# Optimization experiments

Measured on AMD Instinct MI355X. Metric: run time of the kernel, lower is better.

## Reference

```python
import jax, jax.numpy as jnp
import numpy as np

B, L, D, H = 4, 2048, 1024, 16
HD = D // H
EPS_LN = 1e-12
EPS_Z = 1e-6


def _rope_tables(seq_len, d_model, base=10000.0):
    k_max = d_model // 2
    theta = 1.0 / (base ** (np.arange(k_max, dtype=np.float32) / k_max))
    ang = np.arange(seq_len, dtype=np.float32)[:, None] * theta[None, :]  # [L, D/2]
    return jnp.asarray(np.cos(ang)), jnp.asarray(np.sin(ang))


def _apply_rope(x, cos, sin):
    # x: [B, L, D]; complex rotation on (even, odd) pairs of last dim
    xr, xi = x[..., 0::2], x[..., 1::2]          # [B, L, D/2]
    or_ = xr * cos - xi * sin
    oi = xr * sin + xi * cos
    return jnp.stack([or_, oi], axis=-1).reshape(x.shape)


def _layernorm(x, g, b):
    mu = jnp.mean(x, axis=-1, keepdims=True)
    var = jnp.mean(jnp.square(x - mu), axis=-1, keepdims=True)
    return (x - mu) * jax.lax.rsqrt(var + EPS_LN) * g + b


def _heads(t):
    # [B, L, D] -> [B, H, L, HD]
    return t.reshape(B, L, H, HD).transpose(0, 2, 1, 3)


def _attn(x, W_qk, b_qk, conv_w, conv_b, cos, sin):
    # x: [B, L, D] (output of in_proj)
    qk = x @ W_qk + b_qk                                  # [B, L, 2D]
    q = jax.nn.elu(qk[..., :D]) + 1.0
    k = jax.nn.elu(qk[..., D:]) + 1.0
    v = x
    q_rope = _heads(_apply_rope(q, cos, sin))             # [B, H, L, HD]
    k_rope = _heads(_apply_rope(k, cos, sin))
    qh, kh, vh = _heads(q), _heads(k), _heads(v)
    # normalizer: 1 / (q . mean_L(k))
    k_mean = jnp.mean(kh, axis=2)                          # [B, H, HD]
    z = 1.0 / (jnp.einsum('bhld,bhd->bhl', qh, k_mean) + EPS_Z)  # [B, H, L]
    # kv accumulation (global, scaled by 1/L via two L^-0.5 factors)
    kv = jnp.einsum('bhld,bhle->bhde', k_rope, vh) / L     # [B, H, HD, HD]
    out = jnp.einsum('bhld,bhde->bhle', q_rope, kv) * z[..., None]  # [B,H,L,HD]
    out = out.transpose(0, 2, 1, 3).reshape(B, L, D)
    # depthwise causal conv + SiLU on v (left pad k-1=3, keep length L)
    v_t = v.transpose(0, 2, 1)                             # [B, D, L]
    conv = jax.lax.conv_general_dilated(
        v_t, conv_w, window_strides=(1,), padding=[(3, 0)],
        dimension_numbers=('NCH', 'OIH', 'NCH'), feature_group_count=D)
    conv = jax.nn.silu(conv + conv_b[:, None])             # [B, D, L]
    return out + conv.transpose(0, 2, 1)


def setup_inputs() -> dict:
    key = jax.random.key(0)
    ks = jax.random.split(key, 12)
    s = 0.02
    return {
        'x': jax.random.normal(ks[0], (B, L, D), jnp.float32),
        'ln1_g': jnp.ones((D,), jnp.float32), 'ln1_b': jnp.zeros((D,), jnp.float32),
        'ln2_g': jnp.ones((D,), jnp.float32), 'ln2_b': jnp.zeros((D,), jnp.float32),
        'W_act': jax.random.normal(ks[1], (D, D), jnp.float32) * s,
        'b_act': jnp.zeros((D,), jnp.float32),
        'W_in': jax.random.normal(ks[2], (D, D), jnp.float32) * s,
        'b_in': jnp.zeros((D,), jnp.float32),
        'W_qk': jax.random.normal(ks[3], (D, 2 * D), jnp.float32) * s,
        'b_qk': jnp.zeros((2 * D,), jnp.float32),
        'conv_w': jax.random.normal(ks[4], (D, 1, 4), jnp.float32) * 0.25,
        'conv_b': jnp.zeros((D,), jnp.float32),
        'W_out': jax.random.normal(ks[5], (D, D), jnp.float32) * s,
        'b_out': jnp.zeros((D,), jnp.float32),
        'W1': jax.random.normal(ks[6], (D, 4 * D), jnp.float32) * s,
        'b1': jnp.zeros((4 * D,), jnp.float32),
        'W2': jax.random.normal(ks[7], (4 * D, D), jnp.float32) * s,
        'b2': jnp.zeros((D,), jnp.float32),
    }


def reference(x, ln1_g, ln1_b, ln2_g, ln2_b, W_act, b_act, W_in, b_in,
              W_qk, b_qk, conv_w, conv_b, W_out, b_out, W1, b1, W2, b2):
    cos, sin = _rope_tables(L, D)
    shortcut = x
    h = _layernorm(x, ln1_g, ln1_b)
    act_res = jax.nn.silu(h @ W_act + b_act)
    h = h @ W_in + b_in
    h = _attn(h, W_qk, b_qk, conv_w, conv_b, cos, sin)
    h = (h * act_res) @ W_out + b_out
    x = shortcut + h
    m = _layernorm(x, ln2_g, ln2_b)
    m = jax.nn.gelu(m @ W1 + b1, approximate=False) @ W2 + b2
    return x + m
```

## Files before the change

### kernel.cpp

```cpp
#include <hip/hip_runtime.h>
#include <math.h>

typedef unsigned short ushort_t;
typedef __attribute__((ext_vector_type(4))) float f32x4;
typedef __attribute__((ext_vector_type(8))) __bf16 bf16x8;
typedef __attribute__((ext_vector_type(8))) unsigned short u16x8;
typedef __attribute__((ext_vector_type(4))) unsigned short u16x4;

#define DEV __device__ __forceinline__

#define CB 4
#define CL 2048
#define CD 1024
#define CH 16
#define CHD 64
#define CM 8192

DEV float bf2f(ushort_t u) {
  unsigned int x = ((unsigned int)u) << 16;
  return __builtin_bit_cast(float, x);
}
DEV ushort_t f2bf(float f) {
  unsigned int u = __builtin_bit_cast(unsigned int, f);
  u += 0x7FFFu + ((u >> 16) & 1u);
  return (ushort_t)(u >> 16);
}
DEV void gload16(const void* g, void* l) {
  __builtin_amdgcn_global_load_lds((const __attribute__((address_space(1))) void*)g,
                                   (__attribute__((address_space(3))) void*)l, 16, 0, 0);
}
DEV bf16x8 frag64(const ushort_t* s, int row, int slog) {
  int sl = slog ^ (row & 7);
  return __builtin_bit_cast(bf16x8, *reinterpret_cast<const u16x8*>(s + row * 64 + sl * 8));
}

__global__ void k_rope_tables(ushort_t* __restrict__ cosT, ushort_t* __restrict__ sinT) {
  int idx = blockIdx.x * 256 + threadIdx.x;
  int l = idx >> 9, j = idx & 511;
  float theta = powf(10000.0f, -(float)j * (1.0f / 512.0f));
  float ang = (float)l * theta;
  float s, c;
  sincosf(ang, &s, &c);
  cosT[idx] = f2bf(c);
  sinT[idx] = f2bf(s);
}

__global__ void k_transpose_bf16(const float* __restrict__ src, ushort_t* __restrict__ dst,
                                 int R, int C) {
  __shared__ float tile[32][33];
  int c0 = blockIdx.x * 32, r0 = blockIdx.y * 32;
  int tx = threadIdx.x & 31, ty = threadIdx.x >> 5;
#pragma unroll
  for (int i = 0; i < 32; i += 8) tile[ty + i][tx] = src[(size_t)(r0 + ty + i) * C + c0 + tx];
  __syncthreads();
#pragma unroll
  for (int i = 0; i < 32; i += 8) dst[(size_t)(c0 + ty + i) * R + r0 + tx] = f2bf(tile[tx][ty + i]);
}

__global__ __launch_bounds__(256) void k_layernorm(const float* __restrict__ x,
                                                   const float* __restrict__ g,
                                                   const float* __restrict__ b,
                                                   ushort_t* __restrict__ out) {
  int row = blockIdx.x, t = threadIdx.x;
  const float* xr = x + (size_t)row * CD;
  f32x4 v = ((const f32x4*)xr)[t];
  float s = v.x + v.y + v.z + v.w;
  float s2 = v.x * v.x + v.y * v.y + v.z * v.z + v.w * v.w;
#pragma unroll
  for (int off = 32; off >= 1; off >>= 1) {
    s += __shfl_xor(s, off);
    s2 += __shfl_xor(s2, off);
  }
  __shared__ float red[8];
  int lane = t & 63, w = t >> 6;
  if (lane == 0) { red[w] = s; red[w + 4] = s2; }
  __syncthreads();
  s = red[0] + red[1] + red[2] + red[3];
  s2 = red[4] + red[5] + red[6] + red[7];
  float mu = s * (1.0f / CD);
  float var = s2 * (1.0f / CD) - mu * mu;
  float rs = rsqrtf(var + 1e-12f);
  f32x4 gg = ((const f32x4*)g)[t];
  f32x4 bb = ((const f32x4*)b)[t];
  u16x4 o;
  o.x = f2bf((v.x - mu) * rs * gg.x + bb.x);
  o.y = f2bf((v.y - mu) * rs * gg.y + bb.y);
  o.z = f2bf((v.z - mu) * rs * gg.z + bb.z);
  o.w = f2bf((v.w - mu) * rs * gg.w + bb.w);
  ((u16x4*)(out + (size_t)row * CD))[t] = o;
}

enum { EP_PLAIN = 0, EP_SILU = 1, EP_ELU1 = 2, EP_GELU = 3, EP_ADDX = 4 };

template <int EP>
__global__ __launch_bounds__(256, 2) void k_gemm(const ushort_t* __restrict__ A,
                                                 const ushort_t* __restrict__ Bt, int N, int K,
                                                 const float* __restrict__ bias,
                                                 const float* __restrict__ addf,
                                                 float* __restrict__ outf,
                                                 ushort_t* __restrict__ outb) {
  __shared__ __align__(16) ushort_t sA[128 * 64];
  __shared__ __align__(16) ushort_t sB[128 * 64];
  const int t = threadIdx.x;
  const int lane = t & 63;
  const int w = t >> 6;
  const int wr = w >> 1, wc = w & 1;
  const int m0 = blockIdx.y * 128, n0 = blockIdx.x * 128;

  f32x4 acc[4][4];
#pragma unroll
  for (int i = 0; i < 4; ++i)
#pragma unroll
    for (int j = 0; j < 4; ++j) acc[i][j] = f32x4{0.f, 0.f, 0.f, 0.f};

  for (int kt = 0; kt < K; kt += 64) {
#pragma unroll
    for (int i = 0; i < 4; ++i) {
      int c = t + i * 256;
      int row = c >> 3;
      int sl = (c & 7) ^ (row & 7);
      int ldsoff = (w * 64 + i * 256) * 8;
      gload16(A + (size_t)(m0 + row) * K + kt + sl * 8, sA + ldsoff);
      gload16(Bt + (size_t)(n0 + row) * K + kt + sl * 8, sB + ldsoff);
    }
    __syncthreads();
#pragma unroll
    for (int kk = 0; kk < 2; ++kk) {
      int slog = kk * 4 + (lane >> 4);
      bf16x8 af[4], bfr[4];
#pragma unroll
      for (int mi = 0; mi < 4; ++mi) af[mi] = frag64(sA, wr * 64 + mi * 16 + (lane & 15), slog);
#pragma unroll
      for (int ni = 0; ni < 4; ++ni) bfr[ni] = frag64(sB, wc * 64 + ni * 16 + (lane & 15), slog);
#pragma unroll
      for (int mi = 0; mi < 4; ++mi)
#pragma unroll
        for (int ni = 0; ni < 4; ++ni)
          acc[mi][ni] =
              __builtin_amdgcn_mfma_f32_16x16x32_bf16(af[mi], bfr[ni], acc[mi][ni], 0, 0, 0);
    }
    __syncthreads();
  }

#pragma unroll
  for (int mi = 0; mi < 4; ++mi) {
#pragma unroll
    for (int ni = 0; ni < 4; ++ni) {
      int col = n0 + wc * 64 + ni * 16 + (lane & 15);
      float bc = bias[col];
#pragma unroll
      for (int r = 0; r < 4; ++r) {
        int row = m0 + wr * 64 + mi * 16 + (lane >> 4) * 4 + r;
        size_t idx = (size_t)row * N + col;
        float vv = acc[mi][ni][r] + bc;
        if constexpr (EP == EP_PLAIN) {
          outb[idx] = f2bf(vv);
        } else if constexpr (EP == EP_SILU) {
          outb[idx] = f2bf(vv / (1.f + expf(-vv)));
        } else if constexpr (EP == EP_ELU1) {
          outb[idx] = f2bf(vv > 0.f ? vv + 1.f : expf(vv));
        } else if constexpr (EP == EP_GELU) {
          outb[idx] = f2bf(0.5f * vv * (1.f + erff(vv * 0.70710678118654752f)));
        } else {
          outf[idx] = addf[idx] + vv;
        }
      }
    }
  }
}

__global__ __launch_bounds__(256) void k_attn_reduce(const ushort_t* __restrict__ qk,
                                                     const ushort_t* __restrict__ vbf,
                                                     const ushort_t* __restrict__ cosT,
                                                     const ushort_t* __restrict__ sinT,
                                                     float* __restrict__ kvpart,
                                                     float* __restrict__ kmpart) {
  int bh = blockIdx.x >> 2, ls = blockIdx.x & 3;
  int b = bh >> 4, h = bh & 15;
  int t = threadIdx.x, lane = t & 63, w = t >> 6;

  __shared__ float kst[64][68];
  __shared__ __align__(16) ushort_t krT[64 * 64];
  __shared__ __align__(16) ushort_t vT[64 * 64];
  __shared__ float cst[64][32];
  __shared__ float snt[64][32];
  __shared__ float kmp[4][64];

  float kmacc = 0.f;
  f32x4 acc[4];
#pragma unroll
  for (int i = 0; i < 4; ++i) acc[i] = f32x4{0.f, 0.f, 0.f, 0.f};

  for (int c = ls * 8; c < ls * 8 + 8; ++c) {
    int l0 = c * 64;
    for (int idx = t; idx < 4096; idx += 256) {
      int l = idx >> 6, d = idx & 63;
      size_t grow = (size_t)(b * CL + l0 + l);
      float kvv = bf2f(qk[grow * 2048 + 1024 + h * 64 + d]);
      kst[l][d] = kvv;
      kmacc += kvv;
      ushort_t vv = vbf[grow * CD + h * 64 + d];
      int sl = (l >> 3) ^ (d & 7);
      vT[d * 64 + sl * 8 + (l & 7)] = vv;
    }
    for (int idx = t; idx < 2048; idx += 256) {
      int l = idx >> 5, j = idx & 31;
      size_t p = (size_t)(l0 + l) * 512 + h * 32 + j;
      cst[l][j] = bf2f(cosT[p]);
      snt[l][j] = bf2f(sinT[p]);
    }
    __syncthreads();
    for (int idx = t; idx < 4096; idx += 256) {
      int l = idx >> 6, d = idx & 63, j = d >> 1;
      float cc = cst[l][j], sn = snt[l][j];
      float kr = (d & 1) ? (kst[l][d - 1] * sn + kst[l][d] * cc)
                         : (kst[l][d] * cc - kst[l][d + 1] * sn);
      int sl = (l >> 3) ^ (d & 7);
      krT[d * 64 + sl * 8 + (l & 7)] = f2bf(kr);
    }
    __syncthreads();
#pragma unroll
    for (int kk = 0; kk < 2; ++kk) {
      int slog = kk * 4 + (lane >> 4);
      bf16x8 a = frag64(vT, w * 16 + (lane & 15), slog);
#pragma unroll
      for (int ni = 0; ni < 4; ++ni) {
        bf16x8 bb = frag64(krT, ni * 16 + (lane & 15), slog);
        acc[ni] = __builtin_amdgcn_mfma_f32_16x16x32_bf16(a, bb, acc[ni], 0, 0, 0);
      }
    }
    __syncthreads();
  }
  float* kp = kvpart + ((size_t)(bh * 4 + ls)) * 4096;
#pragma unroll
  for (int ni = 0; ni < 4; ++ni) {
    int d = ni * 16 + (lane & 15);
#pragma unroll
    for (int r = 0; r < 4; ++r) {
      int e = w * 16 + (lane >> 4) * 4 + r;
      kp[e * 64 + d] = acc[ni][r];
    }
  }
  kmp[t >> 6][t & 63] = kmacc;
  __syncthreads();
  if (t < 64) kmpart[(bh * 4 + ls) * 64 + t] = kmp[0][t] + kmp[1][t] + kmp[2][t] + kmp[3][t];
}

__global__ void k_kv_reduce(const float* __restrict__ kvpart, const float* __restrict__ kmpart,
                            ushort_t* __restrict__ kvT, float* __restrict__ kmean) {
  int gid = blockIdx.x * 256 + threadIdx.x;
  int bh = gid >> 12, r = gid & 4095;
  float s = 0.f;
#pragma unroll
  for (int ls = 0; ls < 4; ++ls) s += kvpart[((size_t)(bh * 4 + ls)) * 4096 + r];
  kvT[gid] = f2bf(s);
  if (gid < 64 * 64) {
    int bh2 = gid >> 6, d = gid & 63;
    float m = 0.f;
#pragma unroll
    for (int ls = 0; ls < 4; ++ls) m += kmpart[(bh2 * 4 + ls) * 64 + d];
    kmean[gid] = m;
  }
}

__global__ __launch_bounds__(256) void k_attn_out(const ushort_t* __restrict__ qk,
                                                  const ushort_t* __restrict__ kvT,
                                                  const float* __restrict__ kmean,
                                                  const ushort_t* __restrict__ cosT,
                                                  const ushort_t* __restrict__ sinT,
                                                  float* __restrict__ outlin) {
  int bid = blockIdx.x;
  int bh = bid >> 5, lt = bid & 31;
  int b = bh >> 4, h = bh & 15;
  int l0 = lt * 64;
  int t = threadIdx.x, lane = t & 63, w = t >> 6;

  __shared__ float qst[64][68];
  __shared__ __align__(16) ushort_t qrT[64 * 64];
  __shared__ __align__(16) ushort_t kvs[64 * 64];
  __shared__ float cst[64][32];
  __shared__ float snt[64][32];
  __shared__ float kms[64];
  __shared__ float zrow[64];

  if (t < 64) kms[t] = kmean[bh * 64 + t];
  for (int idx = t; idx < 4096; idx += 256) {
    int l = idx >> 6, d = idx & 63;
    qst[l][d] = bf2f(qk[(size_t)(b * CL + l0 + l) * 2048 + h * 64 + d]);
    ushort_t kvv = kvT[(size_t)bh * 4096 + idx];
    int e = idx >> 6, dd = idx & 63;
    int sl = (dd >> 3) ^ (e & 7);
    kvs[e * 64 + sl * 8 + (dd & 7)] = kvv;
  }
  for (int idx = t; idx < 2048; idx += 256) {
    int l = idx >> 5, j = idx & 31;
    size_t p = (size_t)(l0 + l) * 512 + h * 32 + j;
    cst[l][j] = bf2f(cosT[p]);
    snt[l][j] = bf2f(sinT[p]);
  }
  __syncthreads();
  for (int idx = t; idx < 4096; idx += 256) {
    int l = idx >> 6, d = idx & 63, j = d >> 1;
    float cc = cst[l][j], sn = snt[l][j];
    float qr = (d & 1) ? (qst[l][d - 1] * sn + qst[l][d] * cc)
                       : (qst[l][d] * cc - qst[l][d + 1] * sn);
    int sl = (d >> 3) ^ (l & 7);
    qrT[l * 64 + sl * 8 + (d & 7)] = f2bf(qr);
  }
  if (t < 64) {
    float dot = 0.f;
#pragma unroll
    for (int d = 0; d < 64; ++d) dot += qst[t][d] * kms[d];
    zrow[t] = 1.0f / (dot * (1.0f / (float)CL) + 1e-6f);
  }
  __syncthreads();
  f32x4 acc[4];
#pragma unroll
  for (int i = 0; i < 4; ++i) acc[i] = f32x4{0.f, 0.f, 0.f, 0.f};
#pragma unroll
  for (int kk = 0; kk < 2; ++kk) {
    int slog = kk * 4 + (lane >> 4);
    bf16x8 a = frag64(qrT, w * 16 + (lane & 15), slog);
#pragma unroll
    for (int ni = 0; ni < 4; ++ni) {
      bf16x8 bb = frag64(kvs, ni * 16 + (lane & 15), slog);
      acc[ni] = __builtin_amdgcn_mfma_f32_16x16x32_bf16(a, bb, acc[ni], 0, 0, 0);
    }
  }
#pragma unroll
  for (int ni = 0; ni < 4; ++ni) {
    int e = ni * 16 + (lane & 15);
#pragma unroll
    for (int r = 0; r < 4; ++r) {
      int l = w * 16 + (lane >> 4) * 4 + r;
      float val = acc[ni][r] * zrow[l] * (1.0f / (float)CL);
      outlin[(size_t)(b * CL + l0 + l) * CD + h * 64 + e] = val;
    }
  }
}

__global__ void k_conv_mul(const float* __restrict__ outlin, const ushort_t* __restrict__ vbf,
                           const ushort_t* __restrict__ act, const float* __restrict__ convw,
                           const float* __restrict__ convb, ushort_t* __restrict__ A4) {
  int idx = blockIdx.x * 256 + threadIdx.x;
  int d = idx & 1023;
  int bl = idx >> 10;
  int l = bl & 2047;
  float accv = 0.f;
#pragma unroll
  for (int tt = 0; tt < 4; ++tt) {
    int ll = l - 3 + tt;
    if (ll >= 0) accv += bf2f(vbf[(size_t)(bl - 3 + tt) * CD + d]) * convw[d * 4 + tt];
  }
  accv += convb[d];
  accv = accv / (1.f + expf(-accv));
  float a4 = (outlin[idx] + accv) * bf2f(act[idx]);
  A4[idx] = f2bf(a4);
}

extern "C" void kernel_launch(void* const* d_in, const int* in_sizes, int n_in, void* d_out,
                              int out_size, void* d_ws, size_t ws_size, hipStream_t stream) {
  const float* x = (const float*)d_in[0];
  const float* ln1_g = (const float*)d_in[1];
  const float* ln1_b = (const float*)d_in[2];
  const float* ln2_g = (const float*)d_in[3];
  const float* ln2_b = (const float*)d_in[4];
  const float* W_act = (const float*)d_in[5];
  const float* b_act = (const float*)d_in[6];
  const float* W_in = (const float*)d_in[7];
  const float* b_in = (const float*)d_in[8];
  const float* W_qk = (const float*)d_in[9];
  const float* b_qk = (const float*)d_in[10];
  const float* conv_w = (const float*)d_in[11];
  const float* conv_b = (const float*)d_in[12];
  const float* W_out = (const float*)d_in[13];
  const float* b_out = (const float*)d_in[14];
  const float* W1 = (const float*)d_in[15];
  const float* b1 = (const float*)d_in[16];
  const float* W2 = (const float*)d_in[17];
  const float* b2 = (const float*)d_in[18];
  float* out = (float*)d_out;

  char* w = (char*)d_ws;
  size_t off = 0;
  auto alloc = [&](size_t bytes) {
    void* p = (void*)(w + off);
    off += (bytes + 255) & ~(size_t)255;
    return p;
  };
  const size_t MB = 1024 * 1024;
  ushort_t* cosT = (ushort_t*)alloc((size_t)CL * 512 * 2);
  ushort_t* sinT = (ushort_t*)alloc((size_t)CL * 512 * 2);
  ushort_t* WactT = (ushort_t*)alloc((size_t)1024 * 1024 * 2);
  ushort_t* WinT = (ushort_t*)alloc((size_t)1024 * 1024 * 2);
  ushort_t* WqkT = (ushort_t*)alloc((size_t)2048 * 1024 * 2);
  ushort_t* WoutT = (ushort_t*)alloc((size_t)1024 * 1024 * 2);
  ushort_t* W1T = (ushort_t*)alloc((size_t)4096 * 1024 * 2);
  ushort_t* W2T = (ushort_t*)alloc((size_t)1024 * 4096 * 2);
  ushort_t* kvTb = (ushort_t*)alloc((size_t)64 * 4096 * 2);
  float* kmean = (float*)alloc((size_t)64 * 64 * 4);
  float* kvpart = (float*)alloc((size_t)256 * 4096 * 4);
  float* kmpart = (float*)alloc((size_t)256 * 64 * 4);
  float* x2 = (float*)alloc((size_t)CM * CD * 4);
  char* R1 = (char*)alloc(64 * MB);
  ushort_t* hln = (ushort_t*)R1;
  ushort_t* qkb = (ushort_t*)(R1 + 16 * MB);
  ushort_t* actb = (ushort_t*)(R1 + 48 * MB);
  ushort_t* Gb = (ushort_t*)R1;
  ushort_t* vb = (ushort_t*)alloc(16 * MB);
  char* R2 = (char*)alloc(48 * MB);
  float* outlin = (float*)R2;
  ushort_t* A4 = (ushort_t*)(R2 + 32 * MB);
  ushort_t* mln = (ushort_t*)R2;

  (void)in_sizes; (void)n_in; (void)out_size; (void)ws_size;

  k_rope_tables<<<4096, 256, 0, stream>>>(cosT, sinT);
  k_transpose_bf16<<<dim3(32, 32), 256, 0, stream>>>(W_act, WactT, 1024, 1024);
  k_transpose_bf16<<<dim3(32, 32), 256, 0, stream>>>(W_in, WinT, 1024, 1024);
  k_transpose_bf16<<<dim3(64, 32), 256, 0, stream>>>(W_qk, WqkT, 1024, 2048);
  k_transpose_bf16<<<dim3(32, 32), 256, 0, stream>>>(W_out, WoutT, 1024, 1024);
  k_transpose_bf16<<<dim3(128, 32), 256, 0, stream>>>(W1, W1T, 1024, 4096);
  k_transpose_bf16<<<dim3(32, 128), 256, 0, stream>>>(W2, W2T, 4096, 1024);

  k_layernorm<<<CM, 256, 0, stream>>>(x, ln1_g, ln1_b, hln);

  k_gemm<EP_SILU><<<dim3(8, 64), 256, 0, stream>>>(hln, WactT, 1024, 1024, b_act, nullptr, nullptr, actb);
  k_gemm<EP_PLAIN><<<dim3(8, 64), 256, 0, stream>>>(hln, WinT, 1024, 1024, b_in, nullptr, nullptr, vb);
  k_gemm<EP_ELU1><<<dim3(16, 64), 256, 0, stream>>>(vb, WqkT, 2048, 1024, b_qk, nullptr, nullptr, qkb);

  k_attn_reduce<<<256, 256, 0, stream>>>(qkb, vb, cosT, sinT, kvpart, kmpart);
  k_kv_reduce<<<1024, 256, 0, stream>>>(kvpart, kmpart, kvTb, kmean);
  k_attn_out<<<2048, 256, 0, stream>>>(qkb, kvTb, kmean, cosT, sinT, outlin);
  k_conv_mul<<<32768, 256, 0, stream>>>(outlin, vb, actb, conv_w, conv_b, A4);

  k_gemm<EP_ADDX><<<dim3(8, 64), 256, 0, stream>>>(A4, WoutT, 1024, 1024, b_out, x, x2, nullptr);
  k_layernorm<<<CM, 256, 0, stream>>>(x2, ln2_g, ln2_b, mln);
  k_gemm<EP_GELU><<<dim3(32, 64), 256, 0, stream>>>(mln, W1T, 4096, 1024, b1, nullptr, nullptr, Gb);
  k_gemm<EP_ADDX><<<dim3(8, 64), 256, 0, stream>>>(Gb, W2T, 1024, 4096, b2, x2, out, nullptr);
}
```

Before: 493.4 us.

## Fuse act/in/qk GEMMs via precomposed weights and pipeline GEMM loads

Precomposes W_in·W_qk into a single weight and bias so the act, in and qk projections run as one N=4096 GEMM from the layernorm output, with a three-region epilogue (SiLU, plain, ELU+1). This removes the dependent qk GEMM that previously had to wait for the in_proj result. It also replaces the GEMM with a 512-thread 256x128 tile kernel that triple-buffers global-to-LDS loads using vmcnt waits, remaps block IDs into groups of eight, and raises wave priority during MFMA. The cost is an extra weight-composition GEMM in setup, and qk is now computed from a bf16 product of bf16 weights, which changes rounding relative to the two-step path.

Result: slower. 635.4 us (+28.8%).

```diff
diff --git a/kernel.cpp b/kernel.cpp
--- a/kernel.cpp
+++ b/kernel.cpp
@@ -12,8 +12,6 @@
 #define CB 4
 #define CL 2048
 #define CD 1024
-#define CH 16
-#define CHD 64
 #define CM 8192
 
 DEV float bf2f(ushort_t u) {
@@ -37,7 +35,7 @@
 __global__ void k_rope_tables(ushort_t* __restrict__ cosT, ushort_t* __restrict__ sinT) {
   int idx = blockIdx.x * 256 + threadIdx.x;
   int l = idx >> 9, j = idx & 511;
-  float theta = powf(10000.0f, -(float)j * (1.0f / 512.0f));
+  float theta = exp2f(-(float)j * (13.2877123795494f / 512.0f));
   float ang = (float)l * theta;
   float s, c;
   sincosf(ang, &s, &c);
@@ -55,6 +53,35 @@
   __syncthreads();
 #pragma unroll
   for (int i = 0; i < 32; i += 8) dst[(size_t)(c0 + ty + i) * R + r0 + tx] = f2bf(tile[tx][ty + i]);
+}
+
+__global__ void k_cast_bf16(const float* __restrict__ src, ushort_t* __restrict__ dst) {
+  int i = blockIdx.x * 256 + threadIdx.x;
+  f32x4 v = ((const f32x4*)src)[i];
+  u16x4 o;
+  o.x = f2bf(v.x); o.y = f2bf(v.y); o.z = f2bf(v.z); o.w = f2bf(v.w);
+  ((u16x4*)dst)[i] = o;
+}
+
+__global__ void k_prep_bias(const float* __restrict__ b_act, const float* __restrict__ b_in,
+                            const float* __restrict__ b_qk, const ushort_t* __restrict__ WqkT,
+                            float* __restrict__ bf) {
+  int n = blockIdx.x * 256 + threadIdx.x;
+  if (n < 1024) {
+    bf[n] = b_act[n];
+  } else if (n < 2048) {
+    bf[n] = b_in[n - 1024];
+  } else {
+    int np = n - 2048;
+    float s = b_qk[np];
+    const ushort_t* wr = WqkT + (size_t)np * 1024;
+    for (int j = 0; j < 1024; j += 8) {
+      u16x8 wv = *reinterpret_cast<const u16x8*>(wr + j);
+#pragma unroll
+      for (int k2 = 0; k2 < 8; ++k2) s += bf2f(wv[k2]) * b_in[j + k2];
+    }
+    bf[n] = s;
+  }
 }
 
 __global__ __launch_bounds__(256) void k_layernorm(const float* __restrict__ x,
@@ -90,22 +117,51 @@
   ((u16x4*)(out + (size_t)row * CD))[t] = o;
 }
 
-enum { EP_PLAIN = 0, EP_SILU = 1, EP_ELU1 = 2, EP_GELU = 3, EP_ADDX = 4 };
+enum { EP_PLAIN = 0, EP_GELU = 3, EP_ADDX = 4, EP_FUSED1 = 5 };
+
+#define STAGE6(kt_, b_)                                        \
+  {                                                            \
+    const int kt__ = (kt_);                                    \
+    const int bo__ = (b_) * 24576;                             \
+    _Pragma("unroll") for (int i_ = 0; i_ < 4; ++i_)           \
+        gload16(aSrc[i_] + kt__, aDst[i_] + bo__);             \
+    _Pragma("unroll") for (int i_ = 0; i_ < 2; ++i_)           \
+        gload16(bSrc[i_] + kt__, bDst[i_] + bo__);             \
+  }
 
 template <int EP>
-__global__ __launch_bounds__(256, 2) void k_gemm(const ushort_t* __restrict__ A,
-                                                 const ushort_t* __restrict__ Bt, int N, int K,
-                                                 const float* __restrict__ bias,
-                                                 const float* __restrict__ addf,
-                                                 float* __restrict__ outf,
-                                                 ushort_t* __restrict__ outb) {
-  __shared__ __align__(16) ushort_t sA[128 * 64];
-  __shared__ __align__(16) ushort_t sB[128 * 64];
+__global__ __launch_bounds__(512, 2) void k_gemm2(
+    const ushort_t* __restrict__ A, const ushort_t* __restrict__ Bt, int N, int K, int nbx,
+    const float* __restrict__ bias, const float* __restrict__ addf, float* __restrict__ outf,
+    ushort_t* __restrict__ outb, ushort_t* __restrict__ out2, ushort_t* __restrict__ out3) {
+  __shared__ __align__(16) ushort_t smem[3 * 24576];
   const int t = threadIdx.x;
-  const int lane = t & 63;
-  const int w = t >> 6;
+  const int lane = t & 63, w = t >> 6;
   const int wr = w >> 1, wc = w & 1;
-  const int m0 = blockIdx.y * 128, n0 = blockIdx.x * 128;
+  const int lr = lane & 15, lq = lane >> 4;
+
+  int bid = blockIdx.x;
+  int qq = gridDim.x >> 3;
+  int wg = (bid & 7) * qq + (bid >> 3);
+  int by = wg / nbx, bx = wg - by * nbx;
+  const int m0 = by << 8, n0 = bx << 7;
+
+  const ushort_t* aSrc[4];
+  ushort_t* aDst[4];
+#pragma unroll
+  for (int i = 0; i < 4; ++i) {
+    int c = t + i * 512, row = c >> 3, sl = (c & 7) ^ (row & 7);
+    aSrc[i] = A + (size_t)(m0 + row) * K + sl * 8;
+    aDst[i] = smem + (size_t)(w * 64 + i * 512) * 8;
+  }
+  const ushort_t* bSrc[2];
+  ushort_t* bDst[2];
+#pragma unroll
+  for (int i = 0; i < 2; ++i) {
+    int c = t + i * 512, row = c >> 3, sl = (c & 7) ^ (row & 7);
+    bSrc[i] = Bt + (size_t)(n0 + row) * K + sl * 8;
+    bDst[i] = smem + 16384 + (size_t)(w * 64 + i * 512) * 8;
+  }
 
   f32x4 acc[4][4];
 #pragma unroll
@@ -113,25 +169,31 @@
 #pragma unroll
     for (int j = 0; j < 4; ++j) acc[i][j] = f32x4{0.f, 0.f, 0.f, 0.f};
 
-  for (int kt = 0; kt < K; kt += 64) {
-#pragma unroll
-    for (int i = 0; i < 4; ++i) {
-      int c = t + i * 256;
-      int row = c >> 3;
-      int sl = (c & 7) ^ (row & 7);
-      int ldsoff = (w * 64 + i * 256) * 8;
-      gload16(A + (size_t)(m0 + row) * K + kt + sl * 8, sA + ldsoff);
-      gload16(Bt + (size_t)(n0 + row) * K + kt + sl * 8, sB + ldsoff);
-    }
-    __syncthreads();
+  const int NT = K >> 6;
+  STAGE6(0, 0);
+  STAGE6(64, 1);
+  for (int tt = 0; tt < NT; ++tt) {
+    if (tt + 2 < NT) {
+      STAGE6((tt + 2) << 6, (tt + 2) % 3);
+      asm volatile("s_waitcnt vmcnt(12)" ::: "memory");
+    } else if (tt + 1 < NT) {
+      asm volatile("s_waitcnt vmcnt(6)" ::: "memory");
+    } else {
+      asm volatile("s_waitcnt vmcnt(0)" ::: "memory");
+    }
+    __builtin_amdgcn_s_barrier();
+    __builtin_amdgcn_sched_barrier(0);
+    const ushort_t* sA = smem + (tt % 3) * 24576;
+    const ushort_t* sB = sA + 16384;
+    __builtin_amdgcn_s_setprio(1);
 #pragma unroll
     for (int kk = 0; kk < 2; ++kk) {
-      int slog = kk * 4 + (lane >> 4);
+      int slog = kk * 4 + lq;
       bf16x8 af[4], bfr[4];
 #pragma unroll
-      for (int mi = 0; mi < 4; ++mi) af[mi] = frag64(sA, wr * 64 + mi * 16 + (lane & 15), slog);
-#pragma unroll
-      for (int ni = 0; ni < 4; ++ni) bfr[ni] = frag64(sB, wc * 64 + ni * 16 + (lane & 15), slog);
+      for (int mi = 0; mi < 4; ++mi) af[mi] = frag64(sA, wr * 64 + mi * 16 + lr, slog);
+#pragma unroll
+      for (int ni = 0; ni < 4; ++ni) bfr[ni] = frag64(sB, wc * 64 + ni * 16 + lr, slog);
 #pragma unroll
       for (int mi = 0; mi < 4; ++mi)
 #pragma unroll
@@ -139,30 +201,37 @@
           acc[mi][ni] =
               __builtin_amdgcn_mfma_f32_16x16x32_bf16(af[mi], bfr[ni], acc[mi][ni], 0, 0, 0);
     }
-    __syncthreads();
-  }
-
+    __builtin_amdgcn_s_setprio(0);
+    __builtin_amdgcn_sched_barrier(0);
+    __builtin_amdgcn_s_barrier();
+  }
+
+  const int region = n0 >> 10;
 #pragma unroll
   for (int mi = 0; mi < 4; ++mi) {
 #pragma unroll
     for (int ni = 0; ni < 4; ++ni) {
-      int col = n0 + wc * 64 + ni * 16 + (lane & 15);
-      float bc = bias[col];
+      int col = n0 + wc * 64 + ni * 16 + lr;
+      float bc = bias ? bias[col] : 0.0f;
 #pragma unroll
       for (int r = 0; r < 4; ++r) {
-        int row = m0 + wr * 64 + mi * 16 + (lane >> 4) * 4 + r;
-        size_t idx = (size_t)row * N + col;
+        int row = m0 + wr * 64 + mi * 16 + lq * 4 + r;
         float vv = acc[mi][ni][r] + bc;
-        if constexpr (EP == EP_PLAIN) {
-          outb[idx] = f2bf(vv);
-        } else if constexpr (EP == EP_SILU) {
-          outb[idx] = f2bf(vv / (1.f + expf(-vv)));
-        } else if constexpr (EP == EP_ELU1) {
-          outb[idx] = f2bf(vv > 0.f ? vv + 1.f : expf(vv));
+        if constexpr (EP == EP_FUSED1) {
+          if (region == 0) {
+            outb[(size_t)row * 1024 + col] = f2bf(vv / (1.f + expf(-vv)));
+          } else if (region == 1) {
+            out2[(size_t)row * 1024 + (col - 1024)] = f2bf(vv);
+          } else {
+            out3[(size_t)row * 2048 + (col - 2048)] =
+                f2bf(vv > 0.f ? vv + 1.f : expf(vv));
+          }
+        } else if constexpr (EP == EP_PLAIN) {
+          outb[(size_t)row * N + col] = f2bf(vv);
         } else if constexpr (EP == EP_GELU) {
-          outb[idx] = f2bf(0.5f * vv * (1.f + erff(vv * 0.70710678118654752f)));
+          outb[(size_t)row * N + col] = f2bf(0.5f * vv * (1.f + erff(vv * 0.70710678118654752f)));
         } else {
-          outf[idx] = addf[idx] + vv;
+          outf[(size_t)row * N + col] = addf[(size_t)row * N + col] + vv;
         }
       }
     }
@@ -249,7 +318,8 @@
 __global__ void k_kv_reduce(const float* __restrict__ kvpart, const float* __restrict__ kmpart,
                             ushort_t* __restrict__ kvT, float* __restrict__ kmean) {
   int gid = blockIdx.x * 256 + threadIdx.x;
-  int bh = gid >> 12, r = gid & 4095;
+  int bh = gid >> 12;
+  int r = gid & 4095;
   float s = 0.f;
 #pragma unroll
   for (int ls = 0; ls < 4; ++ls) s += kvpart[((size_t)(bh * 4 + ls)) * 4096 + r];
@@ -391,9 +461,10 @@
   const size_t MB = 1024 * 1024;
   ushort_t* cosT = (ushort_t*)alloc((size_t)CL * 512 * 2);
   ushort_t* sinT = (ushort_t*)alloc((size_t)CL * 512 * 2);
-  ushort_t* WactT = (ushort_t*)alloc((size_t)1024 * 1024 * 2);
-  ushort_t* WinT = (ushort_t*)alloc((size_t)1024 * 1024 * 2);
+  ushort_t* WfT = (ushort_t*)alloc((size_t)4096 * 1024 * 2);
   ushort_t* WqkT = (ushort_t*)alloc((size_t)2048 * 1024 * 2);
+  ushort_t* WinB = (ushort_t*)alloc((size_t)1024 * 1024 * 2);
+  float* bfused = (float*)alloc((size_t)4096 * 4);
   ushort_t* WoutT = (ushort_t*)alloc((size_t)1024 * 1024 * 2);
   ushort_t* W1T = (ushort_t*)alloc((size_t)4096 * 1024 * 2);
   ushort_t* W2T = (ushort_t*)alloc((size_t)1024 * 4096 * 2);
@@ -416,26 +487,33 @@
   (void)in_sizes; (void)n_in; (void)out_size; (void)ws_size;
 
   k_rope_tables<<<4096, 256, 0, stream>>>(cosT, sinT);
-  k_transpose_bf16<<<dim3(32, 32), 256, 0, stream>>>(W_act, WactT, 1024, 1024);
-  k_transpose_bf16<<<dim3(32, 32), 256, 0, stream>>>(W_in, WinT, 1024, 1024);
   k_transpose_bf16<<<dim3(64, 32), 256, 0, stream>>>(W_qk, WqkT, 1024, 2048);
+  k_cast_bf16<<<1024, 256, 0, stream>>>(W_in, WinB);
+  k_transpose_bf16<<<dim3(32, 32), 256, 0, stream>>>(W_act, WfT, 1024, 1024);
+  k_transpose_bf16<<<dim3(32, 32), 256, 0, stream>>>(W_in, WfT + (size_t)1024 * 1024, 1024, 1024);
+  k_gemm2<EP_PLAIN><<<dim3(64), 512, 0, stream>>>(WqkT, WinB, 1024, 1024, 8, nullptr, nullptr,
+                                                  nullptr, WfT + (size_t)2048 * 1024, nullptr,
+                                                  nullptr);
+  k_prep_bias<<<16, 256, 0, stream>>>(b_act, b_in, b_qk, WqkT, bfused);
   k_transpose_bf16<<<dim3(32, 32), 256, 0, stream>>>(W_out, WoutT, 1024, 1024);
   k_transpose_bf16<<<dim3(128, 32), 256, 0, stream>>>(W1, W1T, 1024, 4096);
   k_transpose_bf16<<<dim3(32, 128), 256, 0, stream>>>(W2, W2T, 4096, 1024);
 
   k_layernorm<<<CM, 256, 0, stream>>>(x, ln1_g, ln1_b, hln);
 
-  k_gemm<EP_SILU><<<dim3(8, 64), 256, 0, stream>>>(hln, WactT, 1024, 1024, b_act, nullptr, nullptr, actb);
-  k_gemm<EP_PLAIN><<<dim3(8, 64), 256, 0, stream>>>(hln, WinT, 1024, 1024, b_in, nullptr, nullptr, vb);
-  k_gemm<EP_ELU1><<<dim3(16, 64), 256, 0, stream>>>(vb, WqkT, 2048, 1024, b_qk, nullptr, nullptr, qkb);
+  k_gemm2<EP_FUSED1><<<dim3(1024), 512, 0, stream>>>(hln, WfT, 4096, 1024, 32, bfused, nullptr,
+                                                     nullptr, actb, vb, qkb);
 
   k_attn_reduce<<<256, 256, 0, stream>>>(qkb, vb, cosT, sinT, kvpart, kmpart);
   k_kv_reduce<<<1024, 256, 0, stream>>>(kvpart, kmpart, kvTb, kmean);
   k_attn_out<<<2048, 256, 0, stream>>>(qkb, kvTb, kmean, cosT, sinT, outlin);
   k_conv_mul<<<32768, 256, 0, stream>>>(outlin, vb, actb, conv_w, conv_b, A4);
 
-  k_gemm<EP_ADDX><<<dim3(8, 64), 256, 0, stream>>>(A4, WoutT, 1024, 1024, b_out, x, x2, nullptr);
+  k_gemm2<EP_ADDX><<<dim3(256), 512, 0, stream>>>(A4, WoutT, 1024, 1024, 8, b_out, x, x2, nullptr,
+                                                  nullptr, nullptr);
   k_layernorm<<<CM, 256, 0, stream>>>(x2, ln2_g, ln2_b, mln);
-  k_gemm<EP_GELU><<<dim3(32, 64), 256, 0, stream>>>(mln, W1T, 4096, 1024, b1, nullptr, nullptr, Gb);
-  k_gemm<EP_ADDX><<<dim3(8, 64), 256, 0, stream>>>(Gb, W2T, 1024, 4096, b2, x2, out, nullptr);
-}
+  k_gemm2<EP_GELU><<<dim3(1024), 512, 0, stream>>>(mln, W1T, 4096, 1024, 32, b1, nullptr, nullptr,
+                                                   Gb, nullptr, nullptr);
+  k_gemm2<EP_ADDX><<<dim3(256), 512, 0, stream>>>(Gb, W2T, 1024, 4096, 8, b2, x2, out, nullptr,
+                                                  nullptr, nullptr);
+}
```
